# Kernel optimization log

Measured on AMD Instinct MI355X. Metric: run time of the kernel, lower is better.

Reference implementation:

```python
import jax, jax.numpy as jnp
import numpy as np

B, S, HIDDEN = 2, 1024, 2048
N_HEADS, N_KV_HEADS, HEAD_DIM = 32, 8, 64
GROUP = N_HEADS // N_KV_HEADS  # 4
ROPE_THETA = 10000.0


def rotate_half(x):
    half = x.shape[-1] // 2
    return jnp.concatenate((-x[..., half:], x[..., :half]), axis=-1)


def setup_inputs() -> dict:
    key = jax.random.key(0)
    ks = jax.random.split(key, 5)
    hidden_state = jax.random.normal(ks[0], (B, S, HIDDEN), jnp.float32)
    attention_mask = jnp.ones((B, S), jnp.float32)
    # RoPE tables, shape (S, HEAD_DIM)
    inv_freq = 1.0 / (ROPE_THETA ** (jnp.arange(0, HEAD_DIM, 2, dtype=jnp.float32) / HEAD_DIM))
    freqs = jnp.outer(jnp.arange(S, dtype=jnp.float32), inv_freq)
    emb = jnp.concatenate([freqs, freqs], axis=-1)
    cos, sin = jnp.cos(emb), jnp.sin(emb)
    scale = 0.02
    wq = jax.random.normal(ks[1], (HIDDEN, N_HEADS * HEAD_DIM), jnp.float32) * scale
    wk = jax.random.normal(ks[2], (HIDDEN, N_KV_HEADS * HEAD_DIM), jnp.float32) * scale
    wv = jax.random.normal(ks[3], (HIDDEN, N_KV_HEADS * HEAD_DIM), jnp.float32) * scale
    wo = jax.random.normal(ks[4], (N_HEADS * HEAD_DIM, HIDDEN), jnp.float32) * scale
    return {"hidden_state": hidden_state, "attention_mask": attention_mask,
            "cos": cos, "sin": sin, "wq": wq, "wk": wk, "wv": wv, "wo": wo}


def reference(hidden_state, attention_mask, cos, sin, wq, wk, wv, wo):
    b, s, _ = hidden_state.shape

    def split_heads(x):  # (B,S,n*D) -> (n,B,S,D), matching movedim(-2, 0)
        return jnp.moveaxis(x.reshape(b, s, -1, HEAD_DIM), -2, 0)

    q = split_heads(hidden_state @ wq)   # (H, B, S, D)
    k = split_heads(hidden_state @ wk)   # (KV, B, S, D)
    v = split_heads(hidden_state @ wv)   # (KV, B, S, D)

    q = q * cos + rotate_half(q) * sin
    k = k * cos + rotate_half(k) * sin

    # GQA: repeat_interleave K/V heads to match query heads
    k = jnp.repeat(k, GROUP, axis=0)     # (H, B, S, D)
    v = jnp.repeat(v, GROUP, axis=0)

    scores = jnp.einsum('hbqd,hbkd->hbqk', q, k) / jnp.sqrt(jnp.float32(HEAD_DIM))

    # causal + padding mask bias: 0 where tril(mask)==1, -inf elsewhere
    m = jnp.tril(jnp.broadcast_to(attention_mask[:, None, :], (b, s, s)))  # (B,S,S)
    bias = jnp.where((1.0 - m) != 0.0, -jnp.inf, 0.0)
    scores = scores + bias               # (H,B,S,S) + (B,S,S)

    attn = jax.nn.softmax(scores, axis=-1)
    ctx = jnp.einsum('hbqk,hbkd->hbqd', attn, v)
    ctx = jnp.moveaxis(ctx, 0, -2).reshape(b, s, -1)  # (B,S,H*D)
    out = ctx @ wo
    return (out, jnp.swapaxes(attn, 0, 1))  # attention.transpose(0,1) -> (B,H,S,S)
```

## Files before the change

### kernel.cpp

```cpp
#include <hip/hip_runtime.h>


typedef unsigned short u16;
typedef unsigned char  u8;
typedef unsigned int   u32;
typedef __attribute__((ext_vector_type(4))) float  f32x4;
typedef __attribute__((ext_vector_type(8))) __bf16 bf16x8;

static __device__ __forceinline__ u16 f2b(float f) {
  u32 u = __builtin_bit_cast(u32, f);
  u = u + 0x7fffu + ((u >> 16) & 1u);
  return (u16)(u >> 16);
}

#define GLL16(gp, lp)                                                         \
  __builtin_amdgcn_global_load_lds(                                           \
      (__attribute__((address_space(1))) u32*)(gp),                           \
      (__attribute__((address_space(3))) u32*)(lp), 16, 0, 0)

__global__ __launch_bounds__(256) void cvt_kernel(const float* __restrict__ in,
                                                  u16* __restrict__ out, int n4) {
  int i = blockIdx.x * 256 + threadIdx.x;
  if (i >= n4) return;
  float4 v = ((const float4*)in)[i];
  ushort4 o;
  o.x = f2b(v.x); o.y = f2b(v.y); o.z = f2b(v.z); o.w = f2b(v.w);
  ((ushort4*)out)[i] = o;
}

__global__ __launch_bounds__(256) void tconv_kernel(const float* __restrict__ in,
                                                    u16* __restrict__ out,
                                                    int K, int N) {
  __shared__ float t[64][65];
  int k0 = blockIdx.x * 64, n0 = blockIdx.y * 64;
  int c = threadIdx.x & 63, r0 = threadIdx.x >> 6;
#pragma unroll
  for (int i = 0; i < 16; ++i) {
    int r = r0 + i * 4;
    t[r][c] = in[(size_t)(k0 + r) * N + n0 + c];
  }
  __syncthreads();
#pragma unroll
  for (int i = 0; i < 16; ++i) {
    int r = r0 + i * 4;
    out[(size_t)(n0 + r) * K + k0 + c] = f2b(t[c][r]);
  }
}

__global__ __launch_bounds__(256) void vtrans_kernel(const u16* __restrict__ vb,
                                                     u16* __restrict__ vt) {
  __shared__ u16 t[64][65];
  int s0 = blockIdx.x * 64;
  int g = blockIdx.y;
  int b = g >> 3, kvh = g & 7;
  int c = threadIdx.x & 63, r0 = threadIdx.x >> 6;
#pragma unroll
  for (int i = 0; i < 16; ++i) {
    int r = r0 + i * 4;
    t[r][c] = vb[(size_t)(b * 1024 + s0 + r) * 512 + kvh * 64 + c];
  }
  __syncthreads();
#pragma unroll
  for (int i = 0; i < 16; ++i) {
    int r = r0 + i * 4;
    vt[((size_t)g * 64 + r) * 1024 + s0 + c] = t[c][r];
  }
}

template <int EPI>
__global__ __launch_bounds__(256) void gemm_kernel(
    const u16* __restrict__ A, const u16* __restrict__ Bt, int K,
    u16* __restrict__ qb, u16* __restrict__ kb, u16* __restrict__ vb,
    float* __restrict__ out,
    const float* __restrict__ cosT, const float* __restrict__ sinT) {
  __shared__ u16 As[128 * 64];
  __shared__ u16 Bs[128 * 64];
  const int tid = threadIdx.x;
  const int w = tid >> 6, l = tid & 63;
  const int wr = w >> 1, wc = w & 1;
  const int lg = l >> 4, ll = l & 15;
  const int l8 = l >> 3, lc = l & 7;
  const int m0 = blockIdx.x * 128, n0 = blockIdx.y * 128;

  f32x4 acc[4][4] = {};

  const int nkt = K >> 6;
  for (int kt = 0; kt < nkt; ++kt) {
    __syncthreads();
#pragma unroll
    for (int i = 0; i < 4; ++i) {
      int r0 = w * 32 + i * 8;
      int row = r0 + l8;
      int cc = lc ^ (row & 7);
      GLL16(A  + (size_t)(m0 + row) * K + kt * 64 + cc * 8, &As[r0 * 64]);
      GLL16(Bt + (size_t)(n0 + row) * K + kt * 64 + cc * 8, &Bs[r0 * 64]);
    }
    __syncthreads();
#pragma unroll
    for (int kc = 0; kc < 2; ++kc) {
      int cblk = kc * 4 + lg;
      bf16x8 af[4], bfr[4];
#pragma unroll
      for (int mi = 0; mi < 4; ++mi) {
        int row = wr * 64 + mi * 16 + ll;
        af[mi] = *(const bf16x8*)&As[row * 64 + ((cblk ^ (row & 7)) * 8)];
      }
#pragma unroll
      for (int ni = 0; ni < 4; ++ni) {
        int row = wc * 64 + ni * 16 + ll;
        bfr[ni] = *(const bf16x8*)&Bs[row * 64 + ((cblk ^ (row & 7)) * 8)];
      }
#pragma unroll
      for (int mi = 0; mi < 4; ++mi)
#pragma unroll
        for (int ni = 0; ni < 4; ++ni)
          acc[mi][ni] = __builtin_amdgcn_mfma_f32_16x16x32_bf16(
              af[mi], bfr[ni], acc[mi][ni], 0, 0, 0);
    }
  }

  if constexpr (EPI == 0) {
    u16* dst; int ldc, c0;
    const bool dorope = (n0 < 2560);
    if (n0 < 2048)      { dst = qb; ldc = 2048; c0 = n0; }
    else if (n0 < 2560) { dst = kb; ldc = 512;  c0 = n0 - 2048; }
    else                { dst = vb; ldc = 512;  c0 = n0 - 2560; }
#pragma unroll
    for (int mi = 0; mi < 4; ++mi)
#pragma unroll
      for (int ni = 0; ni < 4; ++ni)
#pragma unroll
        for (int r = 0; r < 4; ++r) {
          int row = m0 + wr * 64 + mi * 16 + lg * 4 + r;
          int col = c0 + wc * 64 + ni * 16 + ll;
          float x = acc[mi][ni][r];
          if (dorope) {
            int d = ni * 16 + ll;
            int s = row & 1023;
            float cv = cosT[s * 64 + d], sv = sinT[s * 64 + d];
            float xp = acc[mi][ni ^ 2][r];
            x = (ni < 2) ? (x * cv - xp * sv) : (x * cv + xp * sv);
          }
          dst[(size_t)row * ldc + col] = f2b(x);
        }
  } else {
#pragma unroll
    for (int mi = 0; mi < 4; ++mi)
#pragma unroll
      for (int ni = 0; ni < 4; ++ni)
#pragma unroll
        for (int r = 0; r < 4; ++r) {
          int row = m0 + wr * 64 + mi * 16 + lg * 4 + r;
          int col = n0 + wc * 64 + ni * 16 + ll;
          out[(size_t)row * 2048 + col] = acc[mi][ni][r];
        }
  }
}

__global__ __launch_bounds__(256) void attn_kernel(
    const u16* __restrict__ Qb,
    const u16* __restrict__ Kb,
    const u16* __restrict__ Vt,
    const float* __restrict__ msk,
    float* __restrict__ attn,
    u16* __restrict__ ctx) {
  __shared__ u16 Ks[2][64 * 64];
  __shared__ u16 Vs[2][64 * 64];
  __shared__ float Ps[64 * 68];
  __shared__ u8 Msk[1024];

  const int tid = threadIdx.x, w = tid >> 6, l = tid & 63;
  const int lg = l >> 4, ll = l & 15;
  const int l8 = l >> 3, lc = l & 7;
  const int bid = blockIdx.x;
  const int qt1 = bid & 7;
  const int h = (bid >> 3) & 31;
  const int b = bid >> 8;
  const int kvh = h >> 2;

  for (int i = tid; i < 1024; i += 256) Msk[i] = (msk[b * 1024 + i] != 0.f);

#define STAGE_K(KT, BUF)                                                      \
  {                                                                           \
    for (int j = 0; j < 2; ++j) {                                             \
      int r0 = w * 16 + j * 8;                                                \
      int row = r0 + l8;                                                      \
      int cc = lc ^ (row & 7);                                                \
      GLL16(Kb + (size_t)(b * 1024 + (KT) * 64 + row) * 512 + kvh * 64 +      \
                cc * 8,                                                       \
            &Ks[BUF][r0 * 64]);                                               \
    }                                                                         \
  }
#define STAGE_V(KT, BUF)                                                      \
  {                                                                           \
    for (int j = 0; j < 2; ++j) {                                             \
      int r0 = w * 16 + j * 8;                                                \
      int row = r0 + l8;                                                      \
      int cc = lc ^ (row & 7);                                                \
      GLL16(Vt + (size_t)((b * 8 + kvh) * 64 + row) * 1024 + (KT) * 64 +      \
                cc * 8,                                                       \
            &Vs[BUF][r0 * 64]);                                               \
    }                                                                         \
  }

  for (int half = 0; half < 2; ++half) {
    const int qt = half ? (15 - qt1) : qt1;
    const int qrow0 = qt * 64 + w * 16 + lg * 4;

    bf16x8 qf[2];
    {
      const u16* qp = Qb + (size_t)(b * 1024 + qt * 64 + w * 16 + ll) * 2048 +
                      h * 64 + lg * 8;
      qf[0] = *(const bf16x8*)qp;
      qf[1] = *(const bf16x8*)(qp + 32);
    }

    __syncthreads();
    STAGE_K(0, 0);
    float l_r[4] = {0.f, 0.f, 0.f, 0.f};
    for (int kt = 0; kt <= qt; ++kt) {
      const int c = kt & 1;
      __syncthreads();
      if (kt < qt) STAGE_K(kt + 1, c ^ 1);
      f32x4 sc[4] = {};
#pragma unroll
      for (int kc = 0; kc < 2; ++kc) {
        int cblk = kc * 4 + lg;
#pragma unroll
        for (int ns = 0; ns < 4; ++ns) {
          int row = ns * 16 + ll;
          bf16x8 kf = *(const bf16x8*)&Ks[c][row * 64 + ((cblk ^ (row & 7)) * 8)];
          sc[ns] = __builtin_amdgcn_mfma_f32_16x16x32_bf16(qf[kc], kf, sc[ns], 0, 0, 0);
        }
      }
#pragma unroll
      for (int ns = 0; ns < 4; ++ns) {
        int col = kt * 64 + ns * 16 + ll;
        bool mb = Msk[col];
#pragma unroll
        for (int r = 0; r < 4; ++r) {
          float e = __expf(sc[ns][r] * 0.125f);
          l_r[r] += (mb && col <= qrow0 + r) ? e : 0.f;
        }
      }
    }
#pragma unroll
    for (int r = 0; r < 4; ++r) {
#pragma unroll
      for (int mm = 1; mm < 16; mm <<= 1) l_r[r] += __shfl_xor(l_r[r], mm, 64);
    }
    float rinv[4];
#pragma unroll
    for (int r = 0; r < 4; ++r) rinv[r] = 1.f / l_r[r];

    __syncthreads();
    STAGE_K(0, 0);
    STAGE_V(0, 0);
    f32x4 cacc[4] = {};
    for (int kt = 0; kt <= qt; ++kt) {
      const int c = kt & 1;
      __syncthreads();
      if (kt < qt) { STAGE_K(kt + 1, c ^ 1); STAGE_V(kt + 1, c ^ 1); }
      f32x4 sc[4] = {};
#pragma unroll
      for (int kc = 0; kc < 2; ++kc) {
        int cblk = kc * 4 + lg;
#pragma unroll
        for (int ns = 0; ns < 4; ++ns) {
          int row = ns * 16 + ll;
          bf16x8 kf = *(const bf16x8*)&Ks[c][row * 64 + ((cblk ^ (row & 7)) * 8)];
          sc[ns] = __builtin_amdgcn_mfma_f32_16x16x32_bf16(qf[kc], kf, sc[ns], 0, 0, 0);
        }
      }
#pragma unroll
      for (int ns = 0; ns < 4; ++ns) {
        int col = kt * 64 + ns * 16 + ll;
        bool mb = Msk[col];
#pragma unroll
        for (int r = 0; r < 4; ++r) {
          float e = __expf(sc[ns][r] * 0.125f) * rinv[r];
          float p = (mb && col <= qrow0 + r) ? e : 0.f;
          Ps[(w * 16 + lg * 4 + r) * 68 + ns * 16 + ll] = p;
        }
      }
      {
        size_t rowbase = ((size_t)((b * 32 + h) * 1024 + qt * 64 + w * 16));
#pragma unroll
        for (int rr = 0; rr < 4; ++rr) {
          int lr = rr * 4 + lg;
          f32x4 pv4 = *(const f32x4*)&Ps[(w * 16 + lr) * 68 + ll * 4];
          *(f32x4*)&attn[(rowbase + lr) * 1024 + kt * 64 + ll * 4] = pv4;
        }
      }
#pragma unroll
      for (int kc = 0; kc < 2; ++kc) {
        const float* pp = &Ps[(w * 16 + ll) * 68 + kc * 32 + lg * 8];
        f32x4 plo = *(const f32x4*)pp;
        f32x4 phi = *(const f32x4*)(pp + 4);
        bf16x8 pa;
        pa[0] = (__bf16)plo[0]; pa[1] = (__bf16)plo[1];
        pa[2] = (__bf16)plo[2]; pa[3] = (__bf16)plo[3];
        pa[4] = (__bf16)phi[0]; pa[5] = (__bf16)phi[1];
        pa[6] = (__bf16)phi[2]; pa[7] = (__bf16)phi[3];
        int cblk = kc * 4 + lg;
#pragma unroll
        for (int ns = 0; ns < 4; ++ns) {
          int row = ns * 16 + ll;
          bf16x8 vf = *(const bf16x8*)&Vs[c][row * 64 + ((cblk ^ (row & 7)) * 8)];
          cacc[ns] = __builtin_amdgcn_mfma_f32_16x16x32_bf16(pa, vf, cacc[ns], 0, 0, 0);
        }
      }
    }

#pragma unroll
    for (int ns = 0; ns < 4; ++ns)
#pragma unroll
      for (int r = 0; r < 4; ++r) {
        int tok = b * 1024 + qt * 64 + w * 16 + lg * 4 + r;
        ctx[(size_t)tok * 2048 + h * 64 + ns * 16 + ll] = f2b(cacc[ns][r]);
      }

    int c00 = (qt + 1) * 64;
    int nzf = (1024 - c00) >> 2;
    if (nzf > 0) {
      size_t rb = ((size_t)((b * 32 + h) * 1024 + qt * 64)) * 1024;
      for (int i = tid; i < 64 * nzf; i += 256) {
        int rr = i / nzf;
        int cc4 = i - rr * nzf;
        float4 z = make_float4(0.f, 0.f, 0.f, 0.f);
        *(float4*)&attn[rb + (size_t)rr * 1024 + c00 + (size_t)cc4 * 4] = z;
      }
    }
  }
#undef STAGE_K
#undef STAGE_V
}

extern "C" void kernel_launch(void* const* d_in, const int* in_sizes, int n_in,
                              void* d_out, int out_size, void* d_ws, size_t ws_size,
                              hipStream_t stream) {
  const float* hidden = (const float*)d_in[0];
  const float* mask   = (const float*)d_in[1];
  const float* cosT   = (const float*)d_in[2];
  const float* sinT   = (const float*)d_in[3];
  const float* wq     = (const float*)d_in[4];
  const float* wk     = (const float*)d_in[5];
  const float* wv     = (const float*)d_in[6];
  const float* wo     = (const float*)d_in[7];

  char* ws = (char*)d_ws;
  u16* hidbf = (u16*)(ws);
  u16* Wt    = (u16*)(ws + (8u << 20));
  u16* Qb    = (u16*)(ws + (20u << 20));
  u16* Kb    = (u16*)(ws + (28u << 20));
  u16* Vb    = (u16*)(ws + (30u << 20));
  u16* Vtg   = (u16*)(ws + (32u << 20));

  float* outp  = (float*)d_out;
  float* attnp = outp + (size_t)2 * 1024 * 2048;

  cvt_kernel<<<4096, 256, 0, stream>>>(hidden, hidbf, 1048576);
  tconv_kernel<<<dim3(32, 32), 256, 0, stream>>>(wq, Wt, 2048, 2048);
  tconv_kernel<<<dim3(32, 8), 256, 0, stream>>>(wk, Wt + (size_t)2048 * 2048, 2048, 512);
  tconv_kernel<<<dim3(32, 8), 256, 0, stream>>>(wv, Wt + (size_t)2560 * 2048, 2048, 512);
  gemm_kernel<0><<<dim3(16, 24), 256, 0, stream>>>(hidbf, Wt, 2048, Qb, Kb, Vb,
                                                   nullptr, cosT, sinT);
  vtrans_kernel<<<dim3(16, 16), 256, 0, stream>>>(Vb, Vtg);
  tconv_kernel<<<dim3(32, 32), 256, 0, stream>>>(wo, Wt, 2048, 2048);
  attn_kernel<<<512, 256, 0, stream>>>(Qb, Kb, Vtg, mask, attnp, hidbf);
  gemm_kernel<1><<<dim3(16, 16), 256, 0, stream>>>(hidbf, Wt, 2048,
                                                   nullptr, nullptr, nullptr, outp,
                                                   nullptr, nullptr);
}
```

Baseline: 477.7 us.

## Double-buffer GEMM shared-memory tiles to overlap global loads with MFMA

Shared-memory staging buffers for A and B become two ping-pong buffers. The first k-tile is prefetched before the loop, and each iteration issues the asynchronous global-to-LDS loads for the next tile before running MFMA on the current one. This also removes one barrier per iteration. The aim is to hide global load latency behind matrix math. In exchange, LDS use per block doubles, which may lower occupancy, and the compiler may insert conservative waits that reduce the overlap.

```diff
diff --git a/kernel.cpp b/kernel.cpp
--- a/kernel.cpp
+++ b/kernel.cpp
@@ -73,8 +73,8 @@
     u16* __restrict__ qb, u16* __restrict__ kb, u16* __restrict__ vb,
     float* __restrict__ out,
     const float* __restrict__ cosT, const float* __restrict__ sinT) {
-  __shared__ u16 As[128 * 64];
-  __shared__ u16 Bs[128 * 64];
+  __shared__ u16 As[2][128 * 64];
+  __shared__ u16 Bs[2][128 * 64];
   const int tid = threadIdx.x;
   const int w = tid >> 6, l = tid & 63;
   const int wr = w >> 1, wc = w & 1;
@@ -84,18 +84,26 @@
 
   f32x4 acc[4][4] = {};
 
+#define GSTAGE(KT, BUF)                                                       \
+  {                                                                           \
+    _Pragma("unroll")                                                         \
+    for (int i = 0; i < 4; ++i) {                                             \
+      int r0 = w * 32 + i * 8;                                                \
+      int row = r0 + l8;                                                      \
+      int cc = lc ^ (row & 7);                                                \
+      GLL16(A  + (size_t)(m0 + row) * K + (KT) * 64 + cc * 8,                 \
+            &As[BUF][r0 * 64]);                                               \
+      GLL16(Bt + (size_t)(n0 + row) * K + (KT) * 64 + cc * 8,                 \
+            &Bs[BUF][r0 * 64]);                                               \
+    }                                                                         \
+  }
+
   const int nkt = K >> 6;
+  GSTAGE(0, 0);
+  int cur = 0;
   for (int kt = 0; kt < nkt; ++kt) {
     __syncthreads();
-#pragma unroll
-    for (int i = 0; i < 4; ++i) {
-      int r0 = w * 32 + i * 8;
-      int row = r0 + l8;
-      int cc = lc ^ (row & 7);
-      GLL16(A  + (size_t)(m0 + row) * K + kt * 64 + cc * 8, &As[r0 * 64]);
-      GLL16(Bt + (size_t)(n0 + row) * K + kt * 64 + cc * 8, &Bs[r0 * 64]);
-    }
-    __syncthreads();
+    if (kt + 1 < nkt) GSTAGE(kt + 1, cur ^ 1);
 #pragma unroll
     for (int kc = 0; kc < 2; ++kc) {
       int cblk = kc * 4 + lg;
@@ -103,12 +111,12 @@
 #pragma unroll
       for (int mi = 0; mi < 4; ++mi) {
         int row = wr * 64 + mi * 16 + ll;
-        af[mi] = *(const bf16x8*)&As[row * 64 + ((cblk ^ (row & 7)) * 8)];
+        af[mi] = *(const bf16x8*)&As[cur][row * 64 + ((cblk ^ (row & 7)) * 8)];
       }
 #pragma unroll
       for (int ni = 0; ni < 4; ++ni) {
         int row = wc * 64 + ni * 16 + ll;
-        bfr[ni] = *(const bf16x8*)&Bs[row * 64 + ((cblk ^ (row & 7)) * 8)];
+        bfr[ni] = *(const bf16x8*)&Bs[cur][row * 64 + ((cblk ^ (row & 7)) * 8)];
       }
 #pragma unroll
       for (int mi = 0; mi < 4; ++mi)
@@ -117,7 +125,9 @@
           acc[mi][ni] = __builtin_amdgcn_mfma_f32_16x16x32_bf16(
               af[mi], bfr[ni], acc[mi][ni], 0, 0, 0);
     }
-  }
+    cur ^= 1;
+  }
+#undef GSTAGE
 
   if constexpr (EPI == 0) {
     u16* dst; int ldc, c0;
```

Result: faster. 464.4 us (-2.8%).
